# Kernel tuning notes

Hardware: AMD Instinct MI355X
Metric: run time of the kernel (lower is better)

Reference implementation:

```python
import jax, jax.numpy as jnp
import numpy as np
import math

B, L, C = 4096, 64, 256   # L == window_size
H = 8                     # num_heads
META_H = 384


def _rel_coords_log(W):
    # coords = meshgrid(arange(1), arange(W)) -> (2, W); first row is zeros
    c0 = jnp.zeros((W,), jnp.float32)
    c1 = jnp.arange(W, dtype=jnp.float32)
    coords = jnp.stack([c0, c1], axis=0)                      # (2, W)
    rel = coords[:, :, None] - coords[:, None, :]             # (2, W, W)
    rel = rel.transpose(1, 2, 0).reshape(-1, 2)               # (W*W, 2)
    return jnp.sign(rel) * jnp.log1p(jnp.abs(rel))


def setup_inputs() -> dict:
    key = jax.random.key(0)
    ks = jax.random.split(key, 8)
    s = 0.02
    return {
        "x": jax.random.normal(ks[0], (B, L, C), jnp.float32),
        "qkv_w": jax.random.normal(ks[1], (3 * C, C), jnp.float32) * s,
        "qkv_b": jnp.zeros((3 * C,), jnp.float32),
        "proj_w": jax.random.normal(ks[2], (C, C), jnp.float32) * s,
        "proj_b": jnp.zeros((C,), jnp.float32),
        "logit_scale": jnp.full((H,), math.log(10.0), jnp.float32),
        "mlp1_w": jax.random.normal(ks[3], (META_H, 2), jnp.float32) * s,
        "mlp1_b": jnp.zeros((META_H,), jnp.float32),
        "mlp2_w": jax.random.normal(ks[4], (H, META_H), jnp.float32) * s,
        "mlp2_b": jnp.zeros((H,), jnp.float32),
    }


def reference(x, qkv_w, qkv_b, proj_w, proj_b, logit_scale, mlp1_w, mlp1_b, mlp2_w, mlp2_b):
    b, l, c = x.shape
    h = H
    d = c // h
    qkv = x @ qkv_w.T + qkv_b                                 # (B, L, 3C)
    qkv = qkv.reshape(b, l, 3, h, d).transpose(2, 0, 3, 1, 4) # (3, B, H, L, D)
    q, k, v = qkv[0], qkv[1], qkv[2]
    # cosine attention: L2-normalize q, k (F.normalize, eps=1e-12)
    qn = q / jnp.maximum(jnp.linalg.norm(q, axis=-1, keepdims=True), 1e-12)
    kn = k / jnp.maximum(jnp.linalg.norm(k, axis=-1, keepdims=True), 1e-12)
    attn = jnp.einsum("bhld,bhmd->bhlm", qn, kn)              # (B, H, L, L)
    scale = jnp.exp(jnp.minimum(logit_scale, math.log(1.0 / 0.01)))
    attn = attn * scale.reshape(1, h, 1, 1)
    # MLP relative position bias
    rel = _rel_coords_log(l)                                  # (L*L, 2)
    hid = jax.nn.relu(rel @ mlp1_w.T + mlp1_b)                # (L*L, META_H)
    bias = (hid @ mlp2_w.T + mlp2_b).T.reshape(h, l, l)       # (H, L, L)
    attn = jax.nn.softmax(attn + bias[None], axis=-1)
    out = jnp.einsum("bhlm,bhmd->bhld", attn, v)              # (B, H, L, D)
    out = out.transpose(0, 2, 1, 3).reshape(b, l, c)
    return out @ proj_w.T + proj_b
```

## Files before the change

### kernel.cpp

```cpp
#include <hip/hip_runtime.h>
#include <hip/hip_bf16.h>

typedef __attribute__((ext_vector_type(4))) float f32x4;
typedef __attribute__((ext_vector_type(8))) short short8;
typedef __attribute__((ext_vector_type(4))) short short4_t;

#define LTOK 64
#define CDIM 256
#define FRS 576

static __device__ __forceinline__ short f2bf(float f) {
    __hip_bfloat16 h = __float2bfloat16(f);
    union { __hip_bfloat16 b; short s; } u; u.b = h;
    return u.s;
}
static __device__ __forceinline__ float bf2f(short s) {
    union { unsigned u; float f; } v;
    v.u = ((unsigned)(unsigned short)s) << 16;
    return v.f;
}
static __device__ __forceinline__ int KL(int l) { return l + (l >> 3); }

__global__ void prep_weights(const float* __restrict__ qw, const float* __restrict__ pw,
                             short* __restrict__ wqs, short* __restrict__ wps) {
    int i = blockIdx.x * 256 + threadIdx.x;
    if (i < 768 * 256) {
        int row = i >> 8, col = i & 255;
        int nt = row >> 4, lcr = row & 15;
        int kt = col >> 5, lg = (col >> 3) & 3, j = col & 7;
        wqs[(size_t)(((nt * 8 + kt) * 64) + lg * 16 + lcr) * 8 + j] = f2bf(qw[i]);
    }
    if (i < 256 * 256) {
        int row = i >> 8, col = i & 255;
        int gs = row >> 4, lcr = row & 15;
        int h = col >> 5, lg = (col >> 3) & 3, j = col & 7;
        wps[(size_t)(((gs * 8 + h) * 64) + lg * 16 + lcr) * 8 + j] = f2bf(pw[i]);
    }
}

__global__ void prep_bias(const float* __restrict__ w1, const float* __restrict__ b1,
                          const float* __restrict__ w2, const float* __restrict__ b2,
                          const float* __restrict__ lsc, float* __restrict__ biasT,
                          float* __restrict__ scT) {
    int t = threadIdx.x;
    if (t < 8) scT[t] = expf(fminf(lsc[t], logf(100.0f)));
    if (t < 127) {
        float delta = (float)(t - 63);
        float sg = (delta > 0.f) ? 1.f : ((delta < 0.f) ? -1.f : 0.f);
        float r = sg * log1pf(fabsf(delta));
        float acc[8];
        #pragma unroll
        for (int q = 0; q < 8; ++q) acc[q] = b2[q];
        for (int m = 0; m < 384; ++m) {
            float hid = fmaxf(fmaf(r, w1[m * 2 + 1], b1[m]), 0.f);
            #pragma unroll
            for (int q = 0; q < 8; ++q) acc[q] = fmaf(hid, w2[q * 384 + m], acc[q]);
        }
        #pragma unroll
        for (int q = 0; q < 8; ++q) biasT[q * 127 + t] = acc[q];
    }
}


__global__ void __launch_bounds__(256, 5)
fused_win_attn(const float* __restrict__ x,
               const float* __restrict__ qkv_b,
               const short* __restrict__ wqs,
               const float* __restrict__ biasT,
               const float* __restrict__ scT,
               float* out)
{
    __shared__ short SH[13824];

    const int tid = threadIdx.x;
    const int w  = tid >> 6;
    const int l  = tid & 63;
    const int lg = l >> 4;
    const int lc = l & 15;
    const int li4 = lg * 4;
    const int blk = blockIdx.x;
    const int klb = KL(l) * 8;

    short* QGF = SH;
    short* KGF = SH + 4608;
    short* VTF = SH + 9216;

    short* ao = (short*)(out + (size_t)blk * (LTOK * CDIM) + 8192);

    short8 xf[8];
    {
        const float* xr = x + (size_t)blk * (LTOK * CDIM) + (size_t)(w * 16 + lc) * CDIM + lg * 8;
        #pragma unroll
        for (int kt = 0; kt < 8; ++kt) {
            f32x4 a = *(const f32x4*)(xr + kt * 32);
            f32x4 b = *(const f32x4*)(xr + kt * 32 + 4);
            short8 t;
            t[0]=f2bf(a[0]); t[1]=f2bf(a[1]); t[2]=f2bf(a[2]); t[3]=f2bf(a[3]);
            t[4]=f2bf(b[0]); t[5]=f2bf(b[1]); t[6]=f2bf(b[2]); t[7]=f2bf(b[3]);
            xf[kt] = t;
        }
    }
    const f32x4 fzero = {0.f, 0.f, 0.f, 0.f};
    short8 ones;
    #pragma unroll
    for (int j = 0; j < 8; ++j) ones[j] = (short)0x3F80;

    #pragma unroll 1
    for (int g = 0; g < 4; ++g) {
        #pragma unroll
        for (int sg = 0; sg < 6; ++sg) {
            const int st0 = sg * 2, st1 = sg * 2 + 1;
            const int gnt0 = (st0 >> 2) * 16 + g * 4 + (st0 & 3);
            const int gnt1 = (st1 >> 2) * 16 + g * 4 + (st1 & 3);
            const short* wb0 = wqs + ((size_t)(gnt0 * 8) * 64 + l) * 8;
            const short* wb1 = wqs + ((size_t)(gnt1 * 8) * 64 + l) * 8;
            f32x4 a0 = fzero, a1 = fzero;
            #pragma unroll
            for (int kt = 0; kt < 8; ++kt) {
                short8 Bf0 = *(const short8*)(wb0 + kt * 512);
                short8 Bf1 = *(const short8*)(wb1 + kt * 512);
                a0 = __builtin_amdgcn_mfma_f32_16x16x32_bf16(xf[kt], Bf0, a0, 0, 0, 0);
                a1 = __builtin_amdgcn_mfma_f32_16x16x32_bf16(xf[kt], Bf1, a1, 0, 0, 0);
            }
            #pragma unroll
            for (int e = 0; e < 2; ++e) {
                const int strip = e ? st1 : st0;
                const f32x4 av = e ? a1 : a0;
                const int s = strip >> 2, nt = strip & 3;
                const float bq = qkv_b[s * 256 + g * 64 + nt * 16 + lc];
                if (s < 2) {
                    short* base = (s ? KGF : QGF) + ((nt >> 1) * 4 + w) * FRS;
                    const int lgc = (nt & 1) * 2 + (lc >> 3);
                    #pragma unroll
                    for (int i = 0; i < 4; ++i) {
                        const int l2 = lgc * 16 + li4 + i;
                        base[KL(l2) * 8 + (lc & 7)] = f2bf(av[i] + bq);
                    }
                } else {
                    short* base = VTF + ((w >> 1) * 4 + nt) * FRS;
                    const int l2 = ((w & 1) * 2 + (lg >> 1)) * 16 + lc;
                    short4_t pk;
                    #pragma unroll
                    for (int i = 0; i < 4; ++i) pk[i] = f2bf(av[i] + bq);
                    *(short4_t*)(base + KL(l2) * 8 + (li4 & 7)) = pk;
                }
            }
        }
        __syncthreads();

        short8 Aq0 = *(const short8*)(QGF + (0 * 4 + w) * FRS + klb);
        short8 Aq1 = *(const short8*)(QGF + (1 * 4 + w) * FRS + klb);
        short* PW = QGF + w * FRS;

        #pragma unroll 1
        for (int hh = 0; hh < 2; ++hh) {
            const int h = 2 * g + hh;
            const float sc = scT[h];
            const short8 Aq = hh ? Aq1 : Aq0;
            float qn = 1e-24f;
            #pragma unroll
            for (int j = 0; j < 8; ++j) { float v = bf2f(Aq[j]); qn = fmaf(v, v, qn); }
            qn += __shfl_xor(qn, 16);
            qn += __shfl_xor(qn, 32);
            const float rq = rsqrtf(qn);
            f32x4 pacc[4];
            float invk[4];
            #pragma unroll
            for (int nt = 0; nt < 4; ++nt) {
                short8 Bk = *(const short8*)(KGF + (hh * 4 + nt) * FRS + klb);
                pacc[nt] = __builtin_amdgcn_mfma_f32_16x16x32_bf16(Aq, Bk, fzero, 0, 0, 0);
                float kn = 1e-24f;
                #pragma unroll
                for (int j = 0; j < 8; ++j) { float v = bf2f(Bk[j]); kn = fmaf(v, v, kn); }
                kn += __shfl_xor(kn, 16);
                kn += __shfl_xor(kn, 32);
                invk[nt] = rsqrtf(kn);
            }
            float iq[4];
            #pragma unroll
            for (int i = 0; i < 4; ++i) iq[i] = __shfl(rq, li4 + i, 16) * sc;
            const float* bt = biasT + h * 127 + w * 16 + 63 - lc;
            float p[4][4];
            #pragma unroll
            for (int i = 0; i < 4; ++i)
                #pragma unroll
                for (int nt = 0; nt < 4; ++nt)
                    p[i][nt] = __expf(pacc[nt][i] * iq[i] * invk[nt] + bt[li4 + i - nt * 16]);
            #pragma unroll
            for (int i = 0; i < 4; ++i)
                #pragma unroll
                for (int nt = 0; nt < 4; ++nt) {
                    const int l2 = ((nt & 1) * 2 + (lc >> 3)) * 16 + li4 + i;
                    PW[(nt >> 1) * 4 * FRS + KL(l2) * 8 + (lc & 7)] = f2bf(p[i][nt]);
                }
            f32x4 oacc[2], sacc;
            oacc[0] = fzero; oacc[1] = fzero; sacc = fzero;
            #pragma unroll
            for (int ktp = 0; ktp < 2; ++ktp) {
                short8 Ap = *(const short8*)(PW + ktp * 4 * FRS + klb);
                #pragma unroll
                for (int ndv = 0; ndv < 2; ++ndv) {
                    short8 Bv = *(const short8*)(VTF + (ktp * 4 + hh * 2 + ndv) * FRS + klb);
                    oacc[ndv] = __builtin_amdgcn_mfma_f32_16x16x32_bf16(Ap, Bv, oacc[ndv], 0, 0, 0);
                }
                sacc = __builtin_amdgcn_mfma_f32_16x16x32_bf16(Ap, ones, sacc, 0, 0, 0);
            }
            float rin[4];
            #pragma unroll
            for (int i = 0; i < 4; ++i) rin[i] = 1.f / sacc[i];
            #pragma unroll
            for (int ndv = 0; ndv < 2; ++ndv)
                #pragma unroll
                for (int i = 0; i < 4; ++i)
                    ao[(w * 16 + li4 + i) * 256 + h * 32 + ndv * 16 + lc] = f2bf(oacc[ndv][i] * rin[i]);
        }
        __syncthreads();
    }
}

__global__ void __launch_bounds__(256, 4)
proj_win(const float* __restrict__ proj_b,
         const short* __restrict__ wps,
         float* out)
{
    __shared__ short AF[32 * FRS];

    const int tid = threadIdx.x;
    const int w  = tid >> 6;
    const int l  = tid & 63;
    const int lg = l >> 4;
    const int lc = l & 15;
    const int li4 = lg * 4;
    const int blk = blockIdx.x;
    const int klb = KL(l) * 8;

    const short* ao = (const short*)(out + (size_t)blk * (LTOK * CDIM) + 8192);

    #pragma unroll
    for (int u = 0; u < 8; ++u) {
        const int f = w * 8 + u;
        const int kt = f >> 2, mt = f & 3;
        short8 t = *(const short8*)(ao + (mt * 16 + lc) * 256 + kt * 32 + lg * 8);
        *(short8*)(AF + f * FRS + klb) = t;
    }
    __syncthreads();

    f32x4 accP[4][4];
    #pragma unroll
    for (int a = 0; a < 4; ++a)
        #pragma unroll
        for (int b = 0; b < 4; ++b) accP[a][b] = (f32x4){0,0,0,0};

    #pragma unroll
    for (int kt = 0; kt < 8; ++kt) {
        short8 Aa0 = *(const short8*)(AF + (kt * 4 + 0) * FRS + klb);
        short8 Aa1 = *(const short8*)(AF + (kt * 4 + 1) * FRS + klb);
        short8 Aa2 = *(const short8*)(AF + (kt * 4 + 2) * FRS + klb);
        short8 Aa3 = *(const short8*)(AF + (kt * 4 + 3) * FRS + klb);
        #pragma unroll
        for (int ntl = 0; ntl < 4; ++ntl) {
            short8 Bp = *(const short8*)(wps + ((size_t)((w * 4 + ntl) * 8 + kt) * 64 + l) * 8);
            accP[0][ntl] = __builtin_amdgcn_mfma_f32_16x16x32_bf16(Aa0, Bp, accP[0][ntl], 0, 0, 0);
            accP[1][ntl] = __builtin_amdgcn_mfma_f32_16x16x32_bf16(Aa1, Bp, accP[1][ntl], 0, 0, 0);
            accP[2][ntl] = __builtin_amdgcn_mfma_f32_16x16x32_bf16(Aa2, Bp, accP[2][ntl], 0, 0, 0);
            accP[3][ntl] = __builtin_amdgcn_mfma_f32_16x16x32_bf16(Aa3, Bp, accP[3][ntl], 0, 0, 0);
        }
    }

    float* ob = out + (size_t)blk * (LTOK * CDIM);
    #pragma unroll
    for (int ntl = 0; ntl < 4; ++ntl) {
        const float pb = proj_b[w * 64 + ntl * 16 + lc];
        #pragma unroll
        for (int mt = 0; mt < 4; ++mt)
            #pragma unroll
            for (int i = 0; i < 4; ++i)
                ob[(size_t)(mt * 16 + li4 + i) * 256 + w * 64 + ntl * 16 + lc] = accP[mt][ntl][i] + pb;
    }
}

extern "C" void kernel_launch(void* const* d_in, const int* in_sizes, int n_in,
                              void* d_out, int out_size, void* d_ws, size_t ws_size,
                              hipStream_t stream) {
    const float* x     = (const float*)d_in[0];
    const float* qkvw  = (const float*)d_in[1];
    const float* qkvb  = (const float*)d_in[2];
    const float* projw = (const float*)d_in[3];
    const float* projb = (const float*)d_in[4];
    const float* lsc   = (const float*)d_in[5];
    const float* w1    = (const float*)d_in[6];
    const float* b1    = (const float*)d_in[7];
    const float* w2    = (const float*)d_in[8];
    const float* b2    = (const float*)d_in[9];
    float* out = (float*)d_out;

    short* wqs   = (short*)d_ws;
    short* wps   = (short*)((char*)d_ws + 393216);
    float* biasT = (float*)((char*)d_ws + 524288);
    float* scT   = (float*)((char*)d_ws + 528384);

    const int nwin = in_sizes[0] / (LTOK * CDIM);

    prep_weights<<<768, 256, 0, stream>>>(qkvw, projw, wqs, wps);
    prep_bias<<<1, 128, 0, stream>>>(w1, b1, w2, b2, lsc, biasT, scT);
    fused_win_attn<<<nwin, 256, 0, stream>>>(x, qkvb, wqs, biasT, scT, out);
    proj_win<<<nwin, 256, 0, stream>>>(projb, wps, out);
}
```

Measured before the change: 505.2 us.

## Fuse output projection into attention kernel, keeping attention output in registers

```diff
diff --git a/kernel.cpp b/kernel.cpp
--- a/kernel.cpp
+++ b/kernel.cpp
@@ -62,12 +62,14 @@
 }
 
 
-__global__ void __launch_bounds__(256, 5)
+__global__ void __launch_bounds__(256, 4)
 fused_win_attn(const float* __restrict__ x,
                const float* __restrict__ qkv_b,
                const short* __restrict__ wqs,
+               const short* __restrict__ wps,
                const float* __restrict__ biasT,
                const float* __restrict__ scT,
+               const float* __restrict__ proj_b,
                float* out)
 {
     __shared__ short SH[13824];
@@ -85,8 +87,6 @@
     short* KGF = SH + 4608;
     short* VTF = SH + 9216;
 
-    short* ao = (short*)(out + (size_t)blk * (LTOK * CDIM) + 8192);
-
     short8 xf[8];
     {
         const float* xr = x + (size_t)blk * (LTOK * CDIM) + (size_t)(w * 16 + lc) * CDIM + lg * 8;
@@ -104,6 +104,8 @@
     short8 ones;
     #pragma unroll
     for (int j = 0; j < 8; ++j) ones[j] = (short)0x3F80;
+
+    short8 ao0, ao1, ao2, ao3, ao4, ao5, ao6, ao7;
 
     #pragma unroll 1
     for (int g = 0; g < 4; ++g) {
@@ -205,77 +207,63 @@
                 }
                 sacc = __builtin_amdgcn_mfma_f32_16x16x32_bf16(Ap, ones, sacc, 0, 0, 0);
             }
-            float rin[4];
-            #pragma unroll
-            for (int i = 0; i < 4; ++i) rin[i] = 1.f / sacc[i];
-            #pragma unroll
-            for (int ndv = 0; ndv < 2; ++ndv)
+            short8 aov;
+            #pragma unroll
+            for (int ndv = 0; ndv < 2; ++ndv) {
                 #pragma unroll
                 for (int i = 0; i < 4; ++i)
-                    ao[(w * 16 + li4 + i) * 256 + h * 32 + ndv * 16 + lc] = f2bf(oacc[ndv][i] * rin[i]);
+                    aov[ndv * 4 + i] = f2bf(oacc[ndv][i] * (1.f / sacc[i]));
+            }
+            if (hh == 0) {
+                switch (g) { case 0: ao0 = aov; break; case 1: ao2 = aov; break;
+                             case 2: ao4 = aov; break; default: ao6 = aov; }
+            } else {
+                switch (g) { case 0: ao1 = aov; break; case 1: ao3 = aov; break;
+                             case 2: ao5 = aov; break; default: ao7 = aov; }
+            }
         }
         __syncthreads();
     }
-}
-
-__global__ void __launch_bounds__(256, 4)
-proj_win(const float* __restrict__ proj_b,
-         const short* __restrict__ wps,
-         float* out)
-{
-    __shared__ short AF[32 * FRS];
-
-    const int tid = threadIdx.x;
-    const int w  = tid >> 6;
-    const int l  = tid & 63;
-    const int lg = l >> 4;
-    const int lc = l & 15;
-    const int li4 = lg * 4;
-    const int blk = blockIdx.x;
-    const int klb = KL(l) * 8;
-
-    const short* ao = (const short*)(out + (size_t)blk * (LTOK * CDIM) + 8192);
-
-    #pragma unroll
-    for (int u = 0; u < 8; ++u) {
-        const int f = w * 8 + u;
-        const int kt = f >> 2, mt = f & 3;
-        short8 t = *(const short8*)(ao + (mt * 16 + lc) * 256 + kt * 32 + lg * 8);
-        *(short8*)(AF + f * FRS + klb) = t;
-    }
-    __syncthreads();
-
-    f32x4 accP[4][4];
-    #pragma unroll
-    for (int a = 0; a < 4; ++a)
-        #pragma unroll
-        for (int b = 0; b < 4; ++b) accP[a][b] = (f32x4){0,0,0,0};
-
-    #pragma unroll
-    for (int kt = 0; kt < 8; ++kt) {
-        short8 Aa0 = *(const short8*)(AF + (kt * 4 + 0) * FRS + klb);
-        short8 Aa1 = *(const short8*)(AF + (kt * 4 + 1) * FRS + klb);
-        short8 Aa2 = *(const short8*)(AF + (kt * 4 + 2) * FRS + klb);
-        short8 Aa3 = *(const short8*)(AF + (kt * 4 + 3) * FRS + klb);
-        #pragma unroll
-        for (int ntl = 0; ntl < 4; ++ntl) {
-            short8 Bp = *(const short8*)(wps + ((size_t)((w * 4 + ntl) * 8 + kt) * 64 + l) * 8);
-            accP[0][ntl] = __builtin_amdgcn_mfma_f32_16x16x32_bf16(Aa0, Bp, accP[0][ntl], 0, 0, 0);
-            accP[1][ntl] = __builtin_amdgcn_mfma_f32_16x16x32_bf16(Aa1, Bp, accP[1][ntl], 0, 0, 0);
-            accP[2][ntl] = __builtin_amdgcn_mfma_f32_16x16x32_bf16(Aa2, Bp, accP[2][ntl], 0, 0, 0);
-            accP[3][ntl] = __builtin_amdgcn_mfma_f32_16x16x32_bf16(Aa3, Bp, accP[3][ntl], 0, 0, 0);
-        }
-    }
-
-    float* ob = out + (size_t)blk * (LTOK * CDIM);
-    #pragma unroll
-    for (int ntl = 0; ntl < 4; ++ntl) {
-        const float pb = proj_b[w * 64 + ntl * 16 + lc];
-        #pragma unroll
-        for (int mt = 0; mt < 4; ++mt)
-            #pragma unroll
-            for (int i = 0; i < 4; ++i)
-                ob[(size_t)(mt * 16 + li4 + i) * 256 + w * 64 + ntl * 16 + lc] = accP[mt][ntl][i] + pb;
+
+    {
+        short* PT = SH + w * (2 * FRS);
+        float* ob = out + (size_t)blk * (LTOK * CDIM) + (size_t)(w * 16) * CDIM;
+        #pragma unroll 1
+        for (int half = 0; half < 2; ++half) {
+            f32x4 accP[8];
+            #pragma unroll
+            for (int n = 0; n < 8; ++n) accP[n] = fzero;
+            #pragma unroll
+            for (int kt = 0; kt < 8; ++kt) {
+                short8 aov;
+                switch (kt) {
+                    case 0: aov = ao0; break; case 1: aov = ao1; break;
+                    case 2: aov = ao2; break; case 3: aov = ao3; break;
+                    case 4: aov = ao4; break; case 5: aov = ao5; break;
+                    case 6: aov = ao6; break; default: aov = ao7;
+                }
+                short* pt = PT + (kt & 1) * FRS;
+                #pragma unroll
+                for (int j = 0; j < 8; ++j) {
+                    const int l2 = ((j >> 2) * 2 + (lc >> 3)) * 16 + li4 + (j & 3);
+                    pt[KL(l2) * 8 + (lc & 7)] = aov[j];
+                }
+                short8 Ap = *(const short8*)(pt + klb);
+                #pragma unroll
+                for (int ntl = 0; ntl < 8; ++ntl) {
+                    const int gs = half * 8 + ntl;
+                    short8 Bp = *(const short8*)(wps + ((size_t)((gs * 8 + kt) * 64) + l) * 8);
+                    accP[ntl] = __builtin_amdgcn_mfma_f32_16x16x32_bf16(Ap, Bp, accP[ntl], 0, 0, 0);
+                }
+            }
+            #pragma unroll
+            for (int ntl = 0; ntl < 8; ++ntl) {
+                const float pb = proj_b[half * 128 + ntl * 16 + lc];
+                #pragma unroll
+                for (int i = 0; i < 4; ++i)
+                    ob[(size_t)(li4 + i) * CDIM + half * 128 + ntl * 16 + lc] = accP[ntl][i] + pb;
+            }
+        }
     }
 }
 
@@ -303,6 +291,5 @@
 
     prep_weights<<<768, 256, 0, stream>>>(qkvw, projw, wqs, wps);
     prep_bias<<<1, 128, 0, stream>>>(w1, b1, w2, b2, lsc, biasT, scT);
-    fused_win_attn<<<nwin, 256, 0, stream>>>(x, qkvb, wqs, biasT, scT, out);
-    proj_win<<<nwin, 256, 0, stream>>>(projb, wps, out);
-}
+    fused_win_attn<<<nwin, 256, 0, stream>>>(x, qkvb, wqs, wps, biasT, scT, projb, out);
+}
```

New measurement: 536.3 us. 1.06x slower.
